# Performance work log

Hardware: AMD Instinct MI355X
Metric: run time of the kernel (lower is better)

The kernel has to match this reference:

```python
import jax, jax.numpy as jnp
import numpy as np

T0, T1, DT = 0.0, 2.0, 0.1
N_SEG = 5
REG_FACTOR = 1.0
LN_EPS = 1e-3  # Keras LayerNormalization default epsilon


def setup_inputs() -> dict:
    key = jax.random.key(0)
    ks = jax.random.split(key, 3)
    B, U, H = 16384, 128, 512
    return {
        "x0": jax.random.normal(ks[0], (B, U), dtype=jnp.float32),
        "W1": jax.random.normal(ks[1], (U, H), dtype=jnp.float32) / np.sqrt(U),
        "b1": jnp.zeros((H,), dtype=jnp.float32),
        "gamma": jnp.ones((H,), dtype=jnp.float32),
        "beta": jnp.zeros((H,), dtype=jnp.float32),
        "W2": jax.random.normal(ks[2], (H, U), dtype=jnp.float32) / np.sqrt(H),
        "b2": jnp.zeros((U,), dtype=jnp.float32),
    }


def _mlp(x, W1, b1, gamma, beta, W2, b2):
    # Dense -> LayerNorm -> ReLU -> Dense
    h = x @ W1 + b1
    mu = jnp.mean(h, axis=-1, keepdims=True)
    var = jnp.mean(jnp.square(h - mu), axis=-1, keepdims=True)
    h = (h - mu) * jax.lax.rsqrt(var + LN_EPS) * gamma + beta
    h = jax.nn.relu(h)
    return h @ W2 + b2


def _rk4_integrate(f, x, n_steps, dt):
    def step(x, _):
        k1 = f(x)
        k2 = f(x + 0.5 * dt * k1)
        k3 = f(x + 0.5 * dt * k2)
        k4 = f(x + dt * k3)
        return x + (dt / 6.0) * (k1 + 2.0 * k2 + 2.0 * k3 + k4), None
    x, _ = jax.lax.scan(step, x, None, length=n_steps)
    return x


def reference(x0, W1, b1, gamma, beta, W2, b2):
    f = lambda x: _mlp(x, W1, b1, gamma, beta, W2, b2)
    t_mid = T1 / 2.0                     # integrate [T0, T1/2] first
    n_steps1 = int(round((t_mid - T0) / DT))          # 10 steps
    seg_len = (t_mid - T0) / N_SEG                    # 0.2
    n_steps_seg = int(round(seg_len / DT))            # 2 steps per segment

    x = _rk4_integrate(f, x0, n_steps1, jnp.float32(DT))

    def seg(x, _):
        x = _rk4_integrate(f, x, n_steps_seg, jnp.float32(DT))
        return x, x
    x, xs = jax.lax.scan(seg, x, None, length=N_SEG)  # xs: [N_SEG, B, U]

    pvfs = f(xs.reshape(-1, xs.shape[-1]))            # [N_SEG*B, U]
    a = jnp.abs(pvfs)
    pvf_norms = jnp.sum(a * jax.nn.softmax(a, axis=-1), axis=-1)
    regularization = REG_FACTOR * jnp.mean(pvf_norms)
    return x, regularization
```

## Files before the change

### kernel.cpp

```cpp
#include <hip/hip_runtime.h>
#include <hip/hip_bf16.h>

typedef short bf16x8 __attribute__((ext_vector_type(8)));
typedef float f32x4  __attribute__((ext_vector_type(4)));
typedef unsigned short ushort_t;

#define DT_F     0.1f
#define LN_EPS_F 1e-3f

__device__ __forceinline__ ushort_t f2bf(float v) {
    union { float f; unsigned u; } x; x.f = v;
    unsigned r = x.u + 0x7fffu + ((x.u >> 16) & 1u);
    return (ushort_t)(r >> 16);
}
__device__ __forceinline__ unsigned pk2(float a, float b) {
    unsigned r;
    asm("v_cvt_pk_bf16_f32 %0, %1, %2" : "=v"(r) : "v"(a), "v"(b));
    return r;
}

__global__ __launch_bounds__(256)
void pack_weights(const float* __restrict__ W1, const float* __restrict__ W2,
                  ushort_t* __restrict__ w1p, ushort_t* __restrict__ w2p)
{
    int tid  = blockIdx.x * 256 + threadIdx.x;
    int lane = tid & 63;
    int g = lane >> 4, l15 = lane & 15;
    int fi = tid >> 6;
    bf16x8 hi;
    if (fi < 128) {
        int mh = fi >> 2, ku = fi & 3;
        #pragma unroll
        for (int j = 0; j < 8; ++j) {
            int u = 16 * (2 * ku + (j >> 2)) + 4 * g + (j & 3);
            hi[j] = (short)f2bf(W1[u * 512 + 16 * mh + l15]);
        }
        ((bf16x8*)w1p)[fi * 64 + lane] = hi;
    } else {
        int fj = fi - 128;
        int mu2 = fj >> 4, kh = fj & 15;
        #pragma unroll
        for (int j = 0; j < 8; ++j) {
            int hr = 16 * (2 * kh + (j >> 2)) + 4 * g + (j & 3);
            hi[j] = (short)f2bf(W2[hr * 128 + 16 * mu2 + l15]);
        }
        ((bf16x8*)w2p)[fj * 64 + lane] = hi;
    }
}

__global__ __launch_bounds__(512, 2)
void node_ode(const float* __restrict__ x0,
              const float* __restrict__ gamma, const float* __restrict__ beta,
              const float* __restrict__ b1,    const float* __restrict__ b2,
              const ushort_t* __restrict__ w1p, const ushort_t* __restrict__ w2p,
              float* __restrict__ out, float* __restrict__ regPart)
{
    extern __shared__ char smem[];
    ushort_t* xinh = (ushort_t*)smem;
    ushort_t* hbuf = (ushort_t*)(smem + 8192);
    float*    gbuf = (float*)(smem + 40960);
    float*    b1b  = (float*)(smem + 45056);
    float*    b2b  = (float*)(smem + 47104);
    float*    lnb  = (float*)(smem + 47616);
    float*    rmx  = (float*)(smem + 49664);

    const int t = threadIdx.x, lane = t & 63, w = t >> 6;
    const int g = lane >> 4, l15 = lane & 15;
    const int row0 = blockIdx.x * 32;

    const bf16x8* w1v = (const bf16x8*)w1p;
    const bf16x8* w2v = (const bf16x8*)w2p;

    gbuf[2 * t] = gamma[t]; gbuf[2 * t + 1] = beta[t]; b1b[t] = b1[t];
    if (t < 128) b2b[t] = b2[t];

    bf16x8 W1r[4][4], W2r[16];
    #pragma unroll
    for (int mhi = 0; mhi < 4; ++mhi)
        #pragma unroll
        for (int ku = 0; ku < 4; ++ku)
            W1r[mhi][ku] = w1v[((4 * w + mhi) * 4 + ku) * 64 + lane];
    #pragma unroll
    for (int kh = 0; kh < 16; ++kh)
        W2r[kh] = w2v[(w * 16 + kh) * 64 + lane];

    f32x4 xreg[2], acck[2], kreg[2];
    #pragma unroll
    for (int nb = 0; nb < 2; ++nb) {
        int brow = row0 + 16 * nb + l15;
        int ucol = 16 * w + 4 * g;
        xreg[nb] = *(const f32x4*)&x0[brow * 128 + ucol];
        kreg[nb] = (f32x4)0.0f;
    }
    __syncthreads();

    float regtot = 0.0f;

    auto build_xin = [&](float c) {
        #pragma unroll
        for (int nb = 0; nb < 2; ++nb) {
            f32x4 xv = xreg[nb];
            if (c != 0.0f) xv += kreg[nb] * c;
            unsigned h01 = pk2(xv[0], xv[1]);
            unsigned h23 = pk2(xv[2], xv[3]);
            int off = (((nb * 4 + (w >> 1)) * 2 + (w & 1)) * 64 + lane) * 4;
            *reinterpret_cast<uint2*>(&xinh[off]) = make_uint2(h01, h23);
        }
    };

    auto do_mm1_ln = [&]() {
        f32x4 acc[4][2];
        #pragma unroll
        for (int mhi = 0; mhi < 4; ++mhi) {
            int mh = 4 * w + mhi;
            f32x4 bv = *(const f32x4*)&b1b[16 * mh + 4 * g];
            #pragma unroll
            for (int nb = 0; nb < 2; ++nb) acc[mhi][nb] = bv;
        }
        #pragma unroll
        for (int ku = 0; ku < 4; ++ku) {
            bf16x8 Bh[2];
            #pragma unroll
            for (int nb = 0; nb < 2; ++nb) {
                int base = (((nb * 4 + ku) * 2) * 64 + lane) * 4;
                union { uint2 u2[2]; bf16x8 v; } uu;
                uu.u2[0] = *reinterpret_cast<const uint2*>(&xinh[base]);
                uu.u2[1] = *reinterpret_cast<const uint2*>(&xinh[base + 256]);
                Bh[nb] = uu.v;
            }
            #pragma unroll
            for (int mhi = 0; mhi < 4; ++mhi) {
                #pragma unroll
                for (int nb = 0; nb < 2; ++nb)
                    acc[mhi][nb] = __builtin_amdgcn_mfma_f32_16x16x32_bf16(W1r[mhi][ku], Bh[nb], acc[mhi][nb], 0, 0, 0);
            }
        }
        float s1[2] = {0,0}, s2[2] = {0,0};
        #pragma unroll
        for (int nb = 0; nb < 2; ++nb)
            #pragma unroll
            for (int mhi = 0; mhi < 4; ++mhi)
                #pragma unroll
                for (int r = 0; r < 4; ++r) {
                    float v = acc[mhi][nb][r];
                    s1[nb] += v; s2[nb] = fmaf(v, v, s2[nb]);
                }
        #pragma unroll
        for (int nb = 0; nb < 2; ++nb) {
            s1[nb] += __shfl_xor(s1[nb], 16); s1[nb] += __shfl_xor(s1[nb], 32);
            s2[nb] += __shfl_xor(s2[nb], 16); s2[nb] += __shfl_xor(s2[nb], 32);
        }
        if (lane < 16) {
            #pragma unroll
            for (int nb = 0; nb < 2; ++nb) {
                lnb[((w * 2 + nb) * 16 + l15) * 2 + 0] = s1[nb];
                lnb[((w * 2 + nb) * 16 + l15) * 2 + 1] = s2[nb];
            }
        }
        __syncthreads();
        float mu_[2], rs_[2];
        #pragma unroll
        for (int nb = 0; nb < 2; ++nb) {
            float t1 = 0.f, t2 = 0.f;
            #pragma unroll
            for (int ww = 0; ww < 8; ++ww) {
                t1 += lnb[((ww * 2 + nb) * 16 + l15) * 2 + 0];
                t2 += lnb[((ww * 2 + nb) * 16 + l15) * 2 + 1];
            }
            float m = t1 * (1.0f / 512.0f);
            float var = t2 * (1.0f / 512.0f) - m * m;
            mu_[nb] = m; rs_[nb] = rsqrtf(var + LN_EPS_F);
        }
        #pragma unroll
        for (int khl = 0; khl < 2; ++khl) {
            float2 gp[2][4];
            #pragma unroll
            for (int half = 0; half < 2; ++half) {
                int mh = 4 * w + 2 * khl + half;
                #pragma unroll
                for (int r = 0; r < 4; ++r)
                    gp[half][r] = *(const float2*)&gbuf[(16 * mh + 4 * g + r) * 2];
            }
            #pragma unroll
            for (int nb = 0; nb < 2; ++nb) {
                float v[8];
                #pragma unroll
                for (int half = 0; half < 2; ++half) {
                    int mhi = 2 * khl + half;
                    #pragma unroll
                    for (int r = 0; r < 4; ++r)
                        v[half * 4 + r] = fmaxf(fmaf((acc[mhi][nb][r] - mu_[nb]) * rs_[nb],
                                                     gp[half][r].x, gp[half][r].y), 0.f);
                }
                uint4 q;
                q.x = pk2(v[0], v[1]); q.y = pk2(v[2], v[3]);
                q.z = pk2(v[4], v[5]); q.w = pk2(v[6], v[7]);
                int kh = 2 * w + khl;
                *reinterpret_cast<uint4*>(&hbuf[((kh * 2 + nb) * 64 + lane) * 8]) = q;
            }
        }
    };

    auto do_mm2 = [&]() {
        f32x4 bv = *(const f32x4*)&b2b[16 * w + 4 * g];
        #pragma unroll
        for (int nb = 0; nb < 2; ++nb) kreg[nb] = bv;
        #pragma unroll
        for (int kh = 0; kh < 16; ++kh) {
            bf16x8 Bf[2];
            #pragma unroll
            for (int nb = 0; nb < 2; ++nb)
                Bf[nb] = *(const bf16x8*)&hbuf[((kh * 2 + nb) * 64 + lane) * 8];
            #pragma unroll
            for (int nb = 0; nb < 2; ++nb)
                kreg[nb] = __builtin_amdgcn_mfma_f32_16x16x32_bf16(W2r[kh], Bf[nb], kreg[nb], 0, 0, 0);
        }
    };

    auto f_eval = [&](float c) {
        build_xin(c);
        __syncthreads();
        do_mm1_ln();
        __syncthreads();
        do_mm2();
    };

    auto do_reg = [&]() {
        float amax[2] = {0, 0};
        #pragma unroll
        for (int nb = 0; nb < 2; ++nb)
            #pragma unroll
            for (int r = 0; r < 4; ++r)
                amax[nb] = fmaxf(amax[nb], fabsf(kreg[nb][r]));
        #pragma unroll
        for (int nb = 0; nb < 2; ++nb) {
            amax[nb] = fmaxf(amax[nb], __shfl_xor(amax[nb], 16));
            amax[nb] = fmaxf(amax[nb], __shfl_xor(amax[nb], 32));
        }
        if (lane < 16) {
            #pragma unroll
            for (int nb = 0; nb < 2; ++nb) rmx[(w * 2 + nb) * 16 + l15] = amax[nb];
        }
        __syncthreads();
        float rmax_[2];
        #pragma unroll
        for (int nb = 0; nb < 2; ++nb) {
            float m = rmx[(0 * 2 + nb) * 16 + l15];
            #pragma unroll
            for (int ww = 1; ww < 8; ++ww) m = fmaxf(m, rmx[(ww * 2 + nb) * 16 + l15]);
            rmax_[nb] = m;
        }
        float se[2] = {0, 0}, sa[2] = {0, 0};
        #pragma unroll
        for (int nb = 0; nb < 2; ++nb)
            #pragma unroll
            for (int r = 0; r < 4; ++r) {
                float a = fabsf(kreg[nb][r]);
                float e = __expf(a - rmax_[nb]);
                se[nb] += e; sa[nb] = fmaf(a, e, sa[nb]);
            }
        #pragma unroll
        for (int nb = 0; nb < 2; ++nb) {
            se[nb] += __shfl_xor(se[nb], 16); se[nb] += __shfl_xor(se[nb], 32);
            sa[nb] += __shfl_xor(sa[nb], 16); sa[nb] += __shfl_xor(sa[nb], 32);
        }
        if (lane < 16) {
            #pragma unroll
            for (int nb = 0; nb < 2; ++nb) {
                lnb[((w * 2 + nb) * 16 + l15) * 2 + 0] = se[nb];
                lnb[((w * 2 + nb) * 16 + l15) * 2 + 1] = sa[nb];
            }
        }
        __syncthreads();
        if (w == 0) {
            int nb = g & 1;
            float nse = 0.f, nsa = 0.f;
            #pragma unroll
            for (int ww = 0; ww < 8; ++ww) {
                nse += lnb[((ww * 2 + nb) * 16 + l15) * 2 + 0];
                nsa += lnb[((ww * 2 + nb) * 16 + l15) * 2 + 1];
            }
            float nrm = (lane < 32) ? (nsa / nse) : 0.0f;
            #pragma unroll
            for (int m = 1; m < 64; m <<= 1) nrm += __shfl_xor(nrm, m);
            if (lane == 0) regtot += nrm;
        }
        __syncthreads();
    };

    for (int s = 0; s < 20; ++s) {
        f_eval(0.0f);
        if (s >= 12 && (s & 1) == 0) do_reg();
        #pragma unroll
        for (int nb = 0; nb < 2; ++nb) acck[nb] = kreg[nb];
        f_eval(0.5f * DT_F);
        #pragma unroll
        for (int nb = 0; nb < 2; ++nb) acck[nb] += kreg[nb] * 2.0f;
        f_eval(0.5f * DT_F);
        #pragma unroll
        for (int nb = 0; nb < 2; ++nb) acck[nb] += kreg[nb] * 2.0f;
        f_eval(DT_F);
        #pragma unroll
        for (int nb = 0; nb < 2; ++nb) {
            acck[nb] += kreg[nb];
            xreg[nb] += acck[nb] * (DT_F / 6.0f);
        }
    }
    f_eval(0.0f);
    do_reg();

    #pragma unroll
    for (int nb = 0; nb < 2; ++nb) {
        int brow = row0 + 16 * nb + l15;
        int ucol = 16 * w + 4 * g;
        *(f32x4*)&out[brow * 128 + ucol] = xreg[nb];
    }
    if (t == 0) regPart[blockIdx.x] = regtot;
}

__global__ __launch_bounds__(64)
void finalize_reg(const float* __restrict__ regPart, float* __restrict__ outReg)
{
    int t = threadIdx.x;
    float s = 0.f;
    #pragma unroll
    for (int i = 0; i < 8; ++i) s += regPart[t + 64 * i];
    #pragma unroll
    for (int m = 1; m < 64; m <<= 1) s += __shfl_xor(s, m);
    if (t == 0) outReg[0] = s * (1.0f / (5.0f * 16384.0f));
}

extern "C" void kernel_launch(void* const* d_in, const int* in_sizes, int n_in,
                              void* d_out, int out_size, void* d_ws, size_t ws_size,
                              hipStream_t stream)
{
    (void)in_sizes; (void)n_in; (void)out_size; (void)ws_size;
    const float* x0    = (const float*)d_in[0];
    const float* W1    = (const float*)d_in[1];
    const float* b1    = (const float*)d_in[2];
    const float* gamma = (const float*)d_in[3];
    const float* beta  = (const float*)d_in[4];
    const float* W2    = (const float*)d_in[5];
    const float* b2    = (const float*)d_in[6];
    float* out = (float*)d_out;

    ushort_t* w1p = (ushort_t*)d_ws;
    ushort_t* w2p = w1p + 65536;
    float* regPart = (float*)((char*)d_ws + 262144);

    pack_weights<<<64, 256, 0, stream>>>(W1, W2, w1p, w2p);
    node_ode<<<512, 512, 50688, stream>>>(x0, gamma, beta, b1, b2, w1p, w2p, out, regPart);
    finalize_reg<<<1, 64, 0, stream>>>(regPart, out + 2097152);
}
```

Measured before the change: 437.4 us.

## Split second matmul across K halves with LDS partial-sum exchange

The second matmul is repartitioned so each wave computes two output-column tiles over half of the hidden dimension. Each hidden-activation fragment read from LDS now feeds two MFMAs instead of one, halving LDS traffic in this stage. Partial sums are then exchanged through a new 16 KB LDS buffer, which costs an extra barrier per function evaluation and more shared memory. The LayerNorm and regularization statistics are also stored as packed float2 values.

```diff
diff --git a/kernel.cpp b/kernel.cpp
--- a/kernel.cpp
+++ b/kernel.cpp
@@ -61,11 +61,14 @@
     float*    gbuf = (float*)(smem + 40960);
     float*    b1b  = (float*)(smem + 45056);
     float*    b2b  = (float*)(smem + 47104);
-    float*    lnb  = (float*)(smem + 47616);
+    float2*   lnb  = (float2*)(smem + 47616);
     float*    rmx  = (float*)(smem + 49664);
+    f32x4*    xch  = (f32x4*)(smem + 50688);
 
     const int t = threadIdx.x, lane = t & 63, w = t >> 6;
     const int g = lane >> 4, l15 = lane & 15;
+    const int p = w & 3, kh2 = w >> 2;
+    const int mu2K = 2 * p + kh2;
     const int row0 = blockIdx.x * 32;
 
     const bf16x8* w1v = (const bf16x8*)w1p;
@@ -74,21 +77,23 @@
     gbuf[2 * t] = gamma[t]; gbuf[2 * t + 1] = beta[t]; b1b[t] = b1[t];
     if (t < 128) b2b[t] = b2[t];
 
-    bf16x8 W1r[4][4], W2r[16];
+    bf16x8 W1r[4][4], W2r[2][8];
     #pragma unroll
     for (int mhi = 0; mhi < 4; ++mhi)
         #pragma unroll
         for (int ku = 0; ku < 4; ++ku)
             W1r[mhi][ku] = w1v[((4 * w + mhi) * 4 + ku) * 64 + lane];
     #pragma unroll
-    for (int kh = 0; kh < 16; ++kh)
-        W2r[kh] = w2v[(w * 16 + kh) * 64 + lane];
+    for (int mu = 0; mu < 2; ++mu)
+        #pragma unroll
+        for (int khi = 0; khi < 8; ++khi)
+            W2r[mu][khi] = w2v[((2 * p + mu) * 16 + 8 * kh2 + khi) * 64 + lane];
 
     f32x4 xreg[2], acck[2], kreg[2];
     #pragma unroll
     for (int nb = 0; nb < 2; ++nb) {
         int brow = row0 + 16 * nb + l15;
-        int ucol = 16 * w + 4 * g;
+        int ucol = 16 * mu2K + 4 * g;
         xreg[nb] = *(const f32x4*)&x0[brow * 128 + ucol];
         kreg[nb] = (f32x4)0.0f;
     }
@@ -103,7 +108,7 @@
             if (c != 0.0f) xv += kreg[nb] * c;
             unsigned h01 = pk2(xv[0], xv[1]);
             unsigned h23 = pk2(xv[2], xv[3]);
-            int off = (((nb * 4 + (w >> 1)) * 2 + (w & 1)) * 64 + lane) * 4;
+            int off = (((nb * 4 + p) * 2 + kh2) * 64 + lane) * 4;
             *reinterpret_cast<uint2*>(&xinh[off]) = make_uint2(h01, h23);
         }
     };
@@ -152,10 +157,8 @@
         }
         if (lane < 16) {
             #pragma unroll
-            for (int nb = 0; nb < 2; ++nb) {
-                lnb[((w * 2 + nb) * 16 + l15) * 2 + 0] = s1[nb];
-                lnb[((w * 2 + nb) * 16 + l15) * 2 + 1] = s2[nb];
-            }
+            for (int nb = 0; nb < 2; ++nb)
+                lnb[(w * 2 + nb) * 16 + l15] = make_float2(s1[nb], s2[nb]);
         }
         __syncthreads();
         float mu_[2], rs_[2];
@@ -164,8 +167,8 @@
             float t1 = 0.f, t2 = 0.f;
             #pragma unroll
             for (int ww = 0; ww < 8; ++ww) {
-                t1 += lnb[((ww * 2 + nb) * 16 + l15) * 2 + 0];
-                t2 += lnb[((ww * 2 + nb) * 16 + l15) * 2 + 1];
+                float2 v = lnb[(ww * 2 + nb) * 16 + l15];
+                t1 += v.x; t2 += v.y;
             }
             float m = t1 * (1.0f / 512.0f);
             float var = t2 * (1.0f / 512.0f) - m * m;
@@ -202,18 +205,46 @@
     };
 
     auto do_mm2 = [&]() {
-        f32x4 bv = *(const f32x4*)&b2b[16 * w + 4 * g];
-        #pragma unroll
-        for (int nb = 0; nb < 2; ++nb) kreg[nb] = bv;
-        #pragma unroll
-        for (int kh = 0; kh < 16; ++kh) {
+        f32x4 bv = *(const f32x4*)&b2b[16 * mu2K + 4 * g];
+        f32x4 kp0[2], kp1[2];
+        if (kh2 == 0) {
+            kp0[0] = bv; kp0[1] = bv;
+            kp1[0] = (f32x4)0.0f; kp1[1] = (f32x4)0.0f;
+        } else {
+            kp0[0] = (f32x4)0.0f; kp0[1] = (f32x4)0.0f;
+            kp1[0] = bv; kp1[1] = bv;
+        }
+        #pragma unroll
+        for (int khi = 0; khi < 8; ++khi) {
+            int kh = 8 * kh2 + khi;
             bf16x8 Bf[2];
             #pragma unroll
             for (int nb = 0; nb < 2; ++nb)
                 Bf[nb] = *(const bf16x8*)&hbuf[((kh * 2 + nb) * 64 + lane) * 8];
             #pragma unroll
-            for (int nb = 0; nb < 2; ++nb)
-                kreg[nb] = __builtin_amdgcn_mfma_f32_16x16x32_bf16(W2r[kh], Bf[nb], kreg[nb], 0, 0, 0);
+            for (int nb = 0; nb < 2; ++nb) {
+                kp0[nb] = __builtin_amdgcn_mfma_f32_16x16x32_bf16(W2r[0][khi], Bf[nb], kp0[nb], 0, 0, 0);
+                kp1[nb] = __builtin_amdgcn_mfma_f32_16x16x32_bf16(W2r[1][khi], Bf[nb], kp1[nb], 0, 0, 0);
+            }
+        }
+        if (kh2 == 0) {
+            #pragma unroll
+            for (int nb = 0; nb < 2; ++nb)
+                xch[((p * 2 + 1) * 2 + nb) * 64 + lane] = kp1[nb];
+        } else {
+            #pragma unroll
+            for (int nb = 0; nb < 2; ++nb)
+                xch[((p * 2 + 0) * 2 + nb) * 64 + lane] = kp0[nb];
+        }
+        __syncthreads();
+        if (kh2 == 0) {
+            #pragma unroll
+            for (int nb = 0; nb < 2; ++nb)
+                kreg[nb] = kp0[nb] + xch[((p * 2 + 0) * 2 + nb) * 64 + lane];
+        } else {
+            #pragma unroll
+            for (int nb = 0; nb < 2; ++nb)
+                kreg[nb] = kp1[nb] + xch[((p * 2 + 1) * 2 + nb) * 64 + lane];
         }
     };
 
@@ -266,10 +297,8 @@
         }
         if (lane < 16) {
             #pragma unroll
-            for (int nb = 0; nb < 2; ++nb) {
-                lnb[((w * 2 + nb) * 16 + l15) * 2 + 0] = se[nb];
-                lnb[((w * 2 + nb) * 16 + l15) * 2 + 1] = sa[nb];
-            }
+            for (int nb = 0; nb < 2; ++nb)
+                lnb[(w * 2 + nb) * 16 + l15] = make_float2(se[nb], sa[nb]);
         }
         __syncthreads();
         if (w == 0) {
@@ -277,8 +306,8 @@
             float nse = 0.f, nsa = 0.f;
             #pragma unroll
             for (int ww = 0; ww < 8; ++ww) {
-                nse += lnb[((ww * 2 + nb) * 16 + l15) * 2 + 0];
-                nsa += lnb[((ww * 2 + nb) * 16 + l15) * 2 + 1];
+                float2 v = lnb[(ww * 2 + nb) * 16 + l15];
+                nse += v.x; nsa += v.y;
             }
             float nrm = (lane < 32) ? (nsa / nse) : 0.0f;
             #pragma unroll
@@ -312,7 +341,7 @@
     #pragma unroll
     for (int nb = 0; nb < 2; ++nb) {
         int brow = row0 + 16 * nb + l15;
-        int ucol = 16 * w + 4 * g;
+        int ucol = 16 * mu2K + 4 * g;
         *(f32x4*)&out[brow * 128 + ucol] = xreg[nb];
     }
     if (t == 0) regPart[blockIdx.x] = regtot;
@@ -349,6 +378,6 @@
     float* regPart = (float*)((char*)d_ws + 262144);
 
     pack_weights<<<64, 256, 0, stream>>>(W1, W2, w1p, w2p);
-    node_ode<<<512, 512, 50688, stream>>>(x0, gamma, beta, b1, b2, w1p, w2p, out, regPart);
+    node_ode<<<512, 512, 67072, stream>>>(x0, gamma, beta, b1, b2, w1p, w2p, out, regPart);
     finalize_reg<<<1, 64, 0, stream>>>(regPart, out + 2097152);
 }
```

After: 464.3 us. 1.06x slower.
